# Performance work log

Measured on AMD Instinct MI355X. Metric: run time of the kernel, lower is better.

The kernel has to match this reference:

```python
import jax, jax.numpy as jnp
import numpy as np

HIDDEN = 512
INPUT = 512
BATCH = 16384


def _quant_dequant(w):
    # mirrors torch: scale = max(|w|)/127 + 1e-8; int8 round-clamp; dequantize
    scale = jnp.max(jnp.abs(w)) / 127.0 + 1e-8
    q = jnp.clip(jnp.round(w / scale), -128, 127)
    return q * scale


def setup_inputs() -> dict:
    key = jax.random.key(0)
    ks = jax.random.split(key, 7)
    x = jax.random.normal(ks[0], (BATCH, INPUT), dtype=jnp.float32)
    h_prev = jax.random.normal(ks[1], (BATCH, HIDDEN), dtype=jnp.float32)
    c_prev = jax.random.normal(ks[2], (BATCH, HIDDEN), dtype=jnp.float32)
    w_ih = _quant_dequant(jax.random.normal(ks[3], (4 * HIDDEN, INPUT), dtype=jnp.float32) * 0.05)
    w_hh = _quant_dequant(jax.random.normal(ks[4], (4 * HIDDEN, HIDDEN), dtype=jnp.float32) * 0.05)
    bias_ih = jax.random.normal(ks[5], (4 * HIDDEN,), dtype=jnp.float32) * 0.05
    bias_hh = jax.random.normal(ks[6], (4 * HIDDEN,), dtype=jnp.float32) * 0.05
    return {"x": x, "h_prev": h_prev, "c_prev": c_prev,
            "w_ih": w_ih, "w_hh": w_hh, "bias_ih": bias_ih, "bias_hh": bias_hh}


def reference(x, h_prev, c_prev, w_ih, w_hh, bias_ih, bias_hh):
    # gates: [B, 4H]
    gates = x @ w_ih.T + bias_ih + h_prev @ w_hh.T + bias_hh
    i_g, f_g, g_g, o_g = jnp.split(gates, 4, axis=1)
    i_g = jax.nn.sigmoid(i_g)
    f_g = jax.nn.sigmoid(f_g)
    g_g = jnp.tanh(g_g)
    o_g = jax.nn.sigmoid(o_g)
    c_new = f_g * c_prev + i_g * g_g
    h_new = o_g * jnp.tanh(c_new)
    return (h_new, c_new)
```

## Files before the change

### kernel.cpp

```cpp
#include <hip/hip_runtime.h>


typedef __attribute__((ext_vector_type(4))) int int4v;
typedef __attribute__((ext_vector_type(8))) short short8;
typedef __attribute__((ext_vector_type(4))) float f32x4;
typedef unsigned int u32;
typedef unsigned short u16;
typedef unsigned char u8;

#define BATCH 16384
#define HID 512
#define KTOT 1024
#define BM 256
#define KSTEPS 16
#define TILEA_BYTES 16384
#define TILEW_BYTES 8192
#define NBM 64
#define NBN 16
#define WSA_BYTES ((size_t)NBM * KSTEPS * TILEA_BYTES)
#define WSW_BYTES ((size_t)NBN * KSTEPS * TILEW_BYTES)
#define SCALE_OFF (WSA_BYTES + WSW_BYTES)
#define PART_OFF (SCALE_OFF + 65536)
#define SW_OFF (PART_OFF + 2048)
#define WS_NEEDED (SW_OFF + 64)
#define PACKA_BLOCKS (BATCH / 4)

__device__ __forceinline__ float sigmoidf_(float v) { return 1.0f / (1.0f + __expf(-v)); }
__device__ __forceinline__ float tanhf_(float v) { return 1.0f - 2.0f / (__expf(2.0f * v) + 1.0f); }

__device__ __forceinline__ u32 pack4(float a, float b, float c, float d, float inv) {
    int q0 = (int)rintf(a * inv), q1 = (int)rintf(b * inv);
    int q2 = (int)rintf(c * inv), q3 = (int)rintf(d * inv);
    return (q0 & 255) | ((q1 & 255) << 8) | ((q2 & 255) << 16) | ((q3 & 255) << 24);
}

__global__ __launch_bounds__(256) void pack_a_wmax(
    const float* __restrict__ x, const float* __restrict__ h_prev,
    const float* __restrict__ w_ih, const float* __restrict__ w_hh,
    u8* __restrict__ wsA, float* __restrict__ aScale, float* __restrict__ part)
{
    const u32 t = threadIdx.x;
    if (blockIdx.x >= PACKA_BLOCKS) {
        const u32 b = blockIdx.x - PACKA_BLOCKS;
        const float* src = (b < 256) ? (w_ih + (size_t)b * 4096)
                                     : (w_hh + (size_t)(b - 256) * 4096);
        float am = 0.f;
        const float4* p = (const float4*)src + t;
        #pragma unroll
        for (int j = 0; j < 4; ++j) {
            float4 v = p[j * 256];
            am = fmaxf(am, fmaxf(fmaxf(fabsf(v.x), fabsf(v.y)), fmaxf(fabsf(v.z), fabsf(v.w))));
        }
        #pragma unroll
        for (int o = 32; o >= 1; o >>= 1) am = fmaxf(am, __shfl_xor(am, o, 64));
        __shared__ float red[4];
        if ((t & 63) == 0) red[t >> 6] = am;
        __syncthreads();
        if (t == 0) part[b] = fmaxf(fmaxf(red[0], red[1]), fmaxf(red[2], red[3]));
        return;
    }
    __shared__ float4 stg[4][256];
    const u32 lane = t & 63;
    const u32 wv = t >> 6;
    const u32 m = blockIdx.x * 4 + wv;
    const float4* xr = (const float4*)(x + (size_t)m * 512);
    const float4* hr = (const float4*)(h_prev + (size_t)m * 512);
    float4 v[4];
    v[0] = xr[lane];
    v[1] = xr[lane + 64];
    v[2] = hr[lane];
    v[3] = hr[lane + 64];
    float am = 0.f;
    #pragma unroll
    for (int j = 0; j < 4; ++j)
        am = fmaxf(am, fmaxf(fmaxf(fabsf(v[j].x), fabsf(v[j].y)),
                             fmaxf(fabsf(v[j].z), fabsf(v[j].w))));
    #pragma unroll
    for (int o = 32; o >= 1; o >>= 1) am = fmaxf(am, __shfl_xor(am, o, 64));
    const float inv = (am > 0.f) ? 127.0f / am : 0.f;
    if (lane == 0) aScale[m] = am * (1.0f / 127.0f);

    #pragma unroll
    for (int j = 0; j < 4; ++j)
        stg[wv][j * 64 + (lane ^ ((lane >> 2) & 7))] = v[j];
    u32 wds[4];
    #pragma unroll
    for (int s = 0; s < 4; ++s) {
        float4 w = stg[wv][(4 * lane + s) ^ (lane & 7)];
        wds[s] = pack4(w.x, w.y, w.z, w.w, inv);
    }
    const u32 bm = m >> 8, row = m & 255;
    const u32 ks = lane >> 2, kc = lane & 3;
    const u32 chunk = ((row >> 4) << 6) | (kc << 4) | (row & 15);
    int4v val = {(int)wds[0], (int)wds[1], (int)wds[2], (int)wds[3]};
    *(int4v*)(wsA + (((size_t)bm * KSTEPS + ks) * 1024 + chunk) * 16) = val;
}

__global__ __launch_bounds__(256) void pack_w(
    const float* __restrict__ w_ih, const float* __restrict__ w_hh,
    const float* __restrict__ part, u8* __restrict__ wsW, float* __restrict__ swOut)
{
    const u32 t = threadIdx.x;
    float am = fmaxf(part[t], part[t + 256]);
    #pragma unroll
    for (int o = 32; o >= 1; o >>= 1) am = fmaxf(am, __shfl_xor(am, o, 64));
    __shared__ float red[4];
    if ((t & 63) == 0) red[t >> 6] = am;
    __syncthreads();
    const float wmax = fmaxf(fmaxf(red[0], red[1]), fmaxf(red[2], red[3]));
    const float inv = 127.0f / wmax;
    if (blockIdx.x == 0 && t == 0) *swOut = wmax * (1.0f / 127.0f);

    const u32 widx = blockIdx.x * 256 + t;
    const u32 tile = widx >> 9;
    const u32 ks = tile & 15, bn = tile >> 4;
    const u32 f = (widx >> 6) & 7;
    const u32 cc = f >> 2, g = f & 3;
    const u32 lane = widx & 63;
    const u32 kc = lane >> 4, colin = lane & 15;
    const u32 wr = g * 512 + bn * 32 + cc * 16 + colin;
    const u32 kglob = ks * 64 + kc * 16;
    const float* src = (kglob < 512) ? (w_ih + (size_t)wr * 512 + kglob)
                                     : (w_hh + (size_t)wr * 512 + (kglob - 512));
    u32 wds[4];
    #pragma unroll
    for (int j = 0; j < 4; ++j) {
        float4 v = *((const float4*)src + j);
        wds[j] = pack4(v.x, v.y, v.z, v.w, inv);
    }
    int4v val = {(int)wds[0], (int)wds[1], (int)wds[2], (int)wds[3]};
    *(int4v*)(wsW + (size_t)widx * 16) = val;
}

__global__ __launch_bounds__(256, 2) void lstm_gemm(
    const u8* __restrict__ wsA, const u8* __restrict__ wsW,
    const float* __restrict__ aScale, const float* __restrict__ swPtr,
    const float* __restrict__ c_prev,
    const float* __restrict__ b_ih, const float* __restrict__ b_hh,
    float* __restrict__ h_out, float* __restrict__ c_out)
{
    const int t = threadIdx.x;
    const u32 bid = blockIdx.x;
    const u32 xcd = bid & 7;
    const u32 slot = bid >> 3;
    const int bm = (int)((slot >> 4) * 8 + xcd);
    const int bn = (int)(slot & 15);
    const int n0 = bn * 32;
    const int rowBase = bm * BM;

    const int lane = t & 63;
    const int wv = t >> 6;
    const int colin = lane & 15;
    const int quad = lane >> 4;

    int4v acc[4][2][4];
    #pragma unroll
    for (int rf = 0; rf < 4; ++rf)
        #pragma unroll
        for (int cc = 0; cc < 2; ++cc)
            #pragma unroll
            for (int g = 0; g < 4; ++g)
                acc[rf][cc][g] = (int4v){0, 0, 0, 0};

    const char* gA = (const char*)wsA + (size_t)bm * KSTEPS * TILEA_BYTES
                     + (size_t)(wv * 4) * 1024 + (size_t)lane * 16;
    const char* gW = (const char*)wsW + (size_t)bn * KSTEPS * TILEW_BYTES
                     + (size_t)lane * 16;

#define LOADF(KS, AF, BF)                                                       \
    {                                                                           \
        _Pragma("unroll")                                                       \
        for (int rf = 0; rf < 4; ++rf)                                          \
            AF[rf] = *(const int4v*)(gA + (size_t)(KS) * TILEA_BYTES + rf * 1024); \
        _Pragma("unroll")                                                       \
        for (int f = 0; f < 8; ++f)                                             \
            BF[f] = *(const int4v*)(gW + (size_t)(KS) * TILEW_BYTES + f * 1024);   \
    }

#define COMPUTEF(AF, BF)                                                        \
    {                                                                           \
        _Pragma("unroll")                                                       \
        for (int rf = 0; rf < 4; ++rf)                                          \
            _Pragma("unroll")                                                   \
            for (int cc = 0; cc < 2; ++cc)                                      \
                _Pragma("unroll")                                               \
                for (int g = 0; g < 4; ++g)                                     \
                    acc[rf][cc][g] = __builtin_amdgcn_mfma_i32_16x16x64_i8(     \
                        AF[rf], BF[cc * 4 + g], acc[rf][cc][g], 0, 0, 0);       \
    }

    int4v af0[4], bf0[8], af1[4], bf1[8];
    LOADF(0, af0, bf0);
    #pragma unroll 1
    for (int ks = 0; ks < KSTEPS; ks += 2) {
        LOADF(ks + 1, af1, bf1);
        COMPUTEF(af0, bf0);
        if (ks + 2 < KSTEPS) LOADF(ks + 2, af0, bf0);
        COMPUTEF(af1, bf1);
    }
#undef LOADF
#undef COMPUTEF

    const float sw = *swPtr;
    float rsc[4][4];
    #pragma unroll
    for (int rf = 0; rf < 4; ++rf)
        #pragma unroll
        for (int reg = 0; reg < 4; ++reg)
            rsc[rf][reg] = aScale[rowBase + wv * 64 + rf * 16 + quad * 4 + reg] * sw;

    float bsum[2][4];
    #pragma unroll
    for (int cc = 0; cc < 2; ++cc) {
        const int colg = n0 + cc * 16 + colin;
        #pragma unroll
        for (int g = 0; g < 4; ++g)
            bsum[cc][g] = b_ih[g * 512 + colg] + b_hh[g * 512 + colg];
    }

    #pragma unroll
    for (int rf = 0; rf < 4; ++rf)
        #pragma unroll
        for (int cc = 0; cc < 2; ++cc) {
            const int colg = n0 + cc * 16 + colin;
            #pragma unroll
            for (int reg = 0; reg < 4; ++reg) {
                const int row = rowBase + wv * 64 + rf * 16 + quad * 4 + reg;
                const size_t off = (size_t)row * 512 + colg;
                const float s = rsc[rf][reg];
                const float ig = (float)acc[rf][cc][0][reg] * s + bsum[cc][0];
                const float fg = (float)acc[rf][cc][1][reg] * s + bsum[cc][1];
                const float gg = (float)acc[rf][cc][2][reg] * s + bsum[cc][2];
                const float og = (float)acc[rf][cc][3][reg] * s + bsum[cc][3];
                const float cp = __builtin_nontemporal_load(c_prev + off);
                const float cn = sigmoidf_(fg) * cp + sigmoidf_(ig) * tanhf_(gg);
                const float hn = sigmoidf_(og) * tanhf_(cn);
                __builtin_nontemporal_store(hn, h_out + off);
                __builtin_nontemporal_store(cn, c_out + off);
            }
        }
}

#define LDSK 72
__device__ __forceinline__ u16 f2bf(float f) {
    u32 u = __builtin_bit_cast(u32, f);
    u += 0x7FFFu + ((u >> 16) & 1u);
    return (u16)(u >> 16);
}
__global__ __launch_bounds__(256, 3) void lstm_fused_v1(
    const float* __restrict__ x, const float* __restrict__ h_prev,
    const float* __restrict__ c_prev, const float* __restrict__ w_ih,
    const float* __restrict__ w_hh, const float* __restrict__ b_ih,
    const float* __restrict__ b_hh, float* __restrict__ h_out,
    float* __restrict__ c_out)
{
    __shared__ u16 sA[128][LDSK];
    __shared__ u16 sW[128][LDSK];
    const int t = threadIdx.x;
    const int bn = blockIdx.x & 15, bm = blockIdx.x >> 4;
    const int n0 = bn * 32, rowBase = bm * 128;
    const int srow = t >> 4, scol = t & 15;
    const int lane = t & 63, wv = t >> 6, colin = lane & 15, quad = lane >> 4;
    f32x4 acc[2][2][4];
    #pragma unroll
    for (int rf = 0; rf < 2; ++rf)
        #pragma unroll
        for (int cc = 0; cc < 2; ++cc)
            #pragma unroll
            for (int g = 0; g < 4; ++g) acc[rf][cc][g] = (f32x4){0.f, 0.f, 0.f, 0.f};
    for (int k0 = 0; k0 < KTOT; k0 += 64) {
        const int kk = (k0 < 512) ? k0 : (k0 - 512);
        const float* aSrc = (k0 < 512) ? x : h_prev;
        const float* wSrc = (k0 < 512) ? w_ih : w_hh;
        __syncthreads();
        #pragma unroll
        for (int p = 0; p < 8; ++p) {
            const int r = srow + p * 16;
            const float4 av = *(const float4*)(aSrc + (size_t)(rowBase + r) * 512 + kk + scol * 4);
            ushort4 ap; ap.x = f2bf(av.x); ap.y = f2bf(av.y); ap.z = f2bf(av.z); ap.w = f2bf(av.w);
            *(ushort4*)&sA[r][scol * 4] = ap;
            const int gate = r >> 5, rr = r & 31;
            const float4 wvv = *(const float4*)(wSrc + (size_t)(gate * 512 + n0 + rr) * 512 + kk + scol * 4);
            ushort4 wp; wp.x = f2bf(wvv.x); wp.y = f2bf(wvv.y); wp.z = f2bf(wvv.z); wp.w = f2bf(wvv.w);
            *(ushort4*)&sW[r][scol * 4] = wp;
        }
        __syncthreads();
        #pragma unroll
        for (int ks = 0; ks < 2; ++ks) {
            short8 af[2];
            #pragma unroll
            for (int rf = 0; rf < 2; ++rf)
                af[rf] = *(const short8*)&sA[wv * 32 + rf * 16 + colin][ks * 32 + quad * 8];
            short8 bfr[2][4];
            #pragma unroll
            for (int cc = 0; cc < 2; ++cc)
                #pragma unroll
                for (int g = 0; g < 4; ++g)
                    bfr[cc][g] = *(const short8*)&sW[g * 32 + cc * 16 + colin][ks * 32 + quad * 8];
            #pragma unroll
            for (int rf = 0; rf < 2; ++rf)
                #pragma unroll
                for (int cc = 0; cc < 2; ++cc)
                    #pragma unroll
                    for (int g = 0; g < 4; ++g)
                        acc[rf][cc][g] = __builtin_amdgcn_mfma_f32_16x16x32_bf16(
                            af[rf], bfr[cc][g], acc[rf][cc][g], 0, 0, 0);
        }
    }
    float bsum[2][4];
    #pragma unroll
    for (int cc = 0; cc < 2; ++cc) {
        const int colg = n0 + cc * 16 + colin;
        #pragma unroll
        for (int g = 0; g < 4; ++g) bsum[cc][g] = b_ih[g * 512 + colg] + b_hh[g * 512 + colg];
    }
    #pragma unroll
    for (int rf = 0; rf < 2; ++rf)
        #pragma unroll
        for (int cc = 0; cc < 2; ++cc) {
            const int colg = n0 + cc * 16 + colin;
            #pragma unroll
            for (int reg = 0; reg < 4; ++reg) {
                const int row = rowBase + wv * 32 + rf * 16 + quad * 4 + reg;
                const size_t off = (size_t)row * 512 + colg;
                const float ig = acc[rf][cc][0][reg] + bsum[cc][0];
                const float fg = acc[rf][cc][1][reg] + bsum[cc][1];
                const float gg = acc[rf][cc][2][reg] + bsum[cc][2];
                const float og = acc[rf][cc][3][reg] + bsum[cc][3];
                const float cp = c_prev[off];
                const float cn = sigmoidf_(fg) * cp + sigmoidf_(ig) * tanhf_(gg);
                const float hn = sigmoidf_(og) * tanhf_(cn);
                h_out[off] = hn;
                c_out[off] = cn;
            }
        }
}

extern "C" void kernel_launch(void* const* d_in, const int* in_sizes, int n_in,
                              void* d_out, int out_size, void* d_ws, size_t ws_size,
                              hipStream_t stream) {
    const float* x      = (const float*)d_in[0];
    const float* h_prev = (const float*)d_in[1];
    const float* c_prev = (const float*)d_in[2];
    const float* w_ih   = (const float*)d_in[3];
    const float* w_hh   = (const float*)d_in[4];
    const float* b_ih   = (const float*)d_in[5];
    const float* b_hh   = (const float*)d_in[6];
    float* h_out = (float*)d_out;
    float* c_out = h_out + (size_t)BATCH * HID;

    if (ws_size >= WS_NEEDED) {
        u8* wsA = (u8*)d_ws;
        u8* wsW = (u8*)d_ws + WSA_BYTES;
        float* aScale = (float*)((char*)d_ws + SCALE_OFF);
        float* part   = (float*)((char*)d_ws + PART_OFF);
        float* swOut  = (float*)((char*)d_ws + SW_OFF);
        pack_a_wmax<<<PACKA_BLOCKS + 512, 256, 0, stream>>>(x, h_prev, w_ih, w_hh,
                                                            wsA, aScale, part);
        pack_w<<<512, 256, 0, stream>>>(w_ih, w_hh, part, wsW, swOut);
        lstm_gemm<<<NBM * NBN, 256, 0, stream>>>(wsA, wsW, aScale, swOut, c_prev,
                                                 b_ih, b_hh, h_out, c_out);
    } else {
        lstm_fused_v1<<<128 * 16, 256, 0, stream>>>(x, h_prev, c_prev, w_ih, w_hh,
                                                    b_ih, b_hh, h_out, c_out);
    }
}
```

Before: 218.2 us.

## Stage shared weight tiles into LDS via global_load_lds instead of per-wave global loads

All four waves of a GEMM block previously loaded the same W fragments from global memory on their own. The W panel for the block is now copied into a 64KB LDS buffer with direct global-to-LDS loads, in two halves of 8 K-steps each, and every wave reads its fragments from LDS. This removes the 4x redundant global/L2 traffic for the weight operand. The cost is extra LDS pressure and barrier stalls: the second half is staged with no overlap against compute. A-fragment prefetching also reads slightly past the block's K range on the last iteration.

```diff
diff --git a/kernel.cpp b/kernel.cpp
--- a/kernel.cpp
+++ b/kernel.cpp
@@ -28,6 +28,12 @@
 __device__ __forceinline__ float sigmoidf_(float v) { return 1.0f / (1.0f + __expf(-v)); }
 __device__ __forceinline__ float tanhf_(float v) { return 1.0f - 2.0f / (__expf(2.0f * v) + 1.0f); }
 
+__device__ __forceinline__ void gload_lds16(const void* g, void* l) {
+    __builtin_amdgcn_global_load_lds(
+        (const __attribute__((address_space(1))) u32*)g,
+        (__attribute__((address_space(3))) u32*)l, 16, 0, 0);
+}
+
 __device__ __forceinline__ u32 pack4(float a, float b, float c, float d, float inv) {
     int q0 = (int)rintf(a * inv), q1 = (int)rintf(b * inv);
     int q2 = (int)rintf(c * inv), q3 = (int)rintf(d * inv);
@@ -139,6 +145,8 @@
     const float* __restrict__ b_ih, const float* __restrict__ b_hh,
     float* __restrict__ h_out, float* __restrict__ c_out)
 {
+    __shared__ u8 sW[65536];
+
     const int t = threadIdx.x;
     const u32 bid = blockIdx.x;
     const u32 xcd = bid & 7;
@@ -164,21 +172,22 @@
 
     const char* gA = (const char*)wsA + (size_t)bm * KSTEPS * TILEA_BYTES
                      + (size_t)(wv * 4) * 1024 + (size_t)lane * 16;
-    const char* gW = (const char*)wsW + (size_t)bn * KSTEPS * TILEW_BYTES
-                     + (size_t)lane * 16;
-
-#define LOADF(KS, AF, BF)                                                       \
+    const char* gW = (const char*)wsW + (size_t)bn * KSTEPS * TILEW_BYTES;
+    const char* sWp = (const char*)sW + (size_t)lane * 16;
+
+#define LOADA(KS, AF)                                                           \
     {                                                                           \
         _Pragma("unroll")                                                       \
         for (int rf = 0; rf < 4; ++rf)                                          \
             AF[rf] = *(const int4v*)(gA + (size_t)(KS) * TILEA_BYTES + rf * 1024); \
+    }
+
+#define COMPW(AF, KS7)                                                          \
+    {                                                                           \
+        int4v wf[8];                                                            \
         _Pragma("unroll")                                                       \
         for (int f = 0; f < 8; ++f)                                             \
-            BF[f] = *(const int4v*)(gW + (size_t)(KS) * TILEW_BYTES + f * 1024);   \
-    }
-
-#define COMPUTEF(AF, BF)                                                        \
-    {                                                                           \
+            wf[f] = *(const int4v*)(sWp + (KS7) * TILEW_BYTES + f * 1024);      \
         _Pragma("unroll")                                                       \
         for (int rf = 0; rf < 4; ++rf)                                          \
             _Pragma("unroll")                                                   \
@@ -186,20 +195,45 @@
                 _Pragma("unroll")                                               \
                 for (int g = 0; g < 4; ++g)                                     \
                     acc[rf][cc][g] = __builtin_amdgcn_mfma_i32_16x16x64_i8(     \
-                        AF[rf], BF[cc * 4 + g], acc[rf][cc][g], 0, 0, 0);       \
-    }
-
-    int4v af0[4], bf0[8], af1[4], bf1[8];
-    LOADF(0, af0, bf0);
+                        AF[rf], wf[cc * 4 + g], acc[rf][cc][g], 0, 0, 0);       \
+    }
+
+#define STAGEW(HALF)                                                            \
+    {                                                                           \
+        _Pragma("unroll")                                                       \
+        for (int j = 0; j < 16; ++j)                                            \
+            gload_lds16(gW + (size_t)(HALF) * 65536 + j * 4096 + t * 16,        \
+                        (char*)sW + j * 4096 + t * 16);                         \
+    }
+
+    int4v af0[4], af1[4];
+    LOADA(0, af0);
+    LOADA(1, af1);
+    STAGEW(0);
+    __syncthreads();
+
     #pragma unroll 1
-    for (int ks = 0; ks < KSTEPS; ks += 2) {
-        LOADF(ks + 1, af1, bf1);
-        COMPUTEF(af0, bf0);
-        if (ks + 2 < KSTEPS) LOADF(ks + 2, af0, bf0);
-        COMPUTEF(af1, bf1);
-    }
-#undef LOADF
-#undef COMPUTEF
+    for (int ks = 0; ks < 8; ks += 2) {
+        COMPW(af0, ks);
+        LOADA(ks + 2, af0);
+        COMPW(af1, ks + 1);
+        LOADA(ks + 3, af1);
+    }
+
+    __syncthreads();
+    STAGEW(1);
+    __syncthreads();
+
+    #pragma unroll 1
+    for (int ks = 8; ks < 16; ks += 2) {
+        COMPW(af0, ks & 7);
+        LOADA(ks + 2, af0);
+        COMPW(af1, (ks + 1) & 7);
+        LOADA(ks + 3, af1);
+    }
+#undef LOADA
+#undef COMPW
+#undef STAGEW
 
     const float sw = *swPtr;
     float rsc[4][4];
```

Result: faster. 210.4 us (-3.6%).
